# Kernel optimization log

Hardware: AMD Instinct MI355X
Metric: run time of the kernel (lower is better)

The kernel has to match this reference:

```python
import jax, jax.numpy as jnp
import numpy as np
from jax.scipy.special import logsumexp

EPS = 0.1
MAX_ITER = 100
LOG_SHIFT = 1e-8


def setup_inputs() -> dict:
    key = jax.random.key(0)
    kx, ky = jax.random.split(key)
    x = jax.random.normal(kx, (4, 2048, 64), dtype=jnp.float32)
    y = jax.random.normal(ky, (4, 2048, 64), dtype=jnp.float32)
    return {"x": x, "y": y}


def _cost_matrix(x, y):
    # |x_i - y_j|^2 summed over features; for p=2 use the expanded quadratic form
    # to avoid materializing a [B, P1, P2, D] intermediate.
    x2 = jnp.sum(x * x, axis=-1)  # [B, P1]
    y2 = jnp.sum(y * y, axis=-1)  # [B, P2]
    xy = jnp.einsum('bpd,bqd->bpq', x, y)  # [B, P1, P2]
    return x2[:, :, None] + y2[:, None, :] - 2.0 * xy


def _M(C, u, v):
    # M_ij = (-C_ij + u_i + v_j) / eps
    return (-C + u[..., :, None] + v[..., None, :]) / EPS


def reference(x, y):
    C = _cost_matrix(x, y)  # [B, P1, P2]
    B, P1, P2 = C.shape
    mu = jnp.full((B, P1), 1.0 / P1, dtype=C.dtype)
    nu = jnp.full((B, P2), 1.0 / P2, dtype=C.dtype)
    log_mu = jnp.log(mu + LOG_SHIFT)
    log_nu = jnp.log(nu + LOG_SHIFT)

    def step(carry, _):
        u, v = carry
        u = EPS * (log_mu - logsumexp(_M(C, u, v), axis=-1)) + u
        # logsumexp of M^T over its last dim == logsumexp of M over axis -2
        v = EPS * (log_nu - logsumexp(_M(C, u, v), axis=-2)) + v
        return (u, v), None

    u0 = jnp.zeros_like(mu)
    v0 = jnp.zeros_like(nu)
    (u, v), _ = jax.lax.scan(step, (u0, v0), None, length=MAX_ITER)

    pi = jnp.exp(_M(C, u, v))  # transport plan [B, P1, P2]
    cost = jnp.sum(pi * C, axis=(-2, -1))  # [B], reduction='none'
    return cost, pi, C
```

## Files before the change

kernel.cpp:

```cpp
#include <hip/hip_runtime.h>
#include <hip/hip_bf16.h>
#include <math.h>


#define P 2048
#define D 64
#define B 4
#define EPS 0.1f
#define KS 14.426950408889634f
#define EL2 0.06931471805599453f

#define EX2 __builtin_amdgcn_exp2f
#define LG2 __builtin_amdgcn_logf

__global__ __launch_bounds__(256) void cost_kernel(
    const float* __restrict__ X, const float* __restrict__ Y,
    float* __restrict__ C) {
  __shared__ float xs[64][65];
  __shared__ float ys[64][65];
  const int b = blockIdx.z;
  const int i0 = blockIdx.y * 64;
  const int j0 = blockIdx.x * 64;
  const float* Xb = X + ((size_t)b * P + i0) * D;
  const float* Yb = Y + ((size_t)b * P + j0) * D;
  const int t = threadIdx.x;
#pragma unroll
  for (int n = 0; n < 4; n++) {
    int e4 = t + n * 256;
    float4 xv = ((const float4*)Xb)[e4];
    float4 yv = ((const float4*)Yb)[e4];
    int r = e4 >> 4;
    int k = (e4 & 15) * 4;
    xs[r][k] = xv.x; xs[r][k + 1] = xv.y; xs[r][k + 2] = xv.z; xs[r][k + 3] = xv.w;
    ys[r][k] = yv.x; ys[r][k + 1] = yv.y; ys[r][k + 2] = yv.z; ys[r][k + 3] = yv.w;
  }
  __syncthreads();
  const int tx = t & 15;
  const int ty = t >> 4;
  float acc[4][4] = {};
#pragma unroll
  for (int k = 0; k < D; k++) {
    float a[4], bb[4];
#pragma unroll
    for (int r = 0; r < 4; r++) a[r] = xs[ty * 4 + r][k];
#pragma unroll
    for (int c = 0; c < 4; c++) bb[c] = ys[tx * 4 + c][k];
#pragma unroll
    for (int r = 0; r < 4; r++)
#pragma unroll
      for (int c = 0; c < 4; c++) {
        float d = a[r] - bb[c];
        acc[r][c] = fmaf(d, d, acc[r][c]);
      }
  }
#pragma unroll
  for (int r = 0; r < 4; r++) {
    float4 o = make_float4(acc[r][0], acc[r][1], acc[r][2], acc[r][3]);
    *(float4*)&C[((size_t)b * P + i0 + ty * 4 + r) * P + j0 + tx * 4] = o;
  }
}

__global__ __launch_bounds__(256, 2) void sweep_kernel(
    const float* __restrict__ C, const float* __restrict__ v,
    float* __restrict__ u, float2* __restrict__ part, float elog) {
  const int bid = blockIdx.x;
  const int grow0 = bid * 16;
  const int b = grow0 >> 11;
  const int kb = bid & 127;
  const int t = threadIdx.x;
  const int lane = t & 63;
  const int w = t >> 6;

  float vvK[8];
  {
    const float4* vp = (const float4*)(v + ((size_t)b << 11) + t * 8);
    float4 a = vp[0], c4 = vp[1];
    vvK[0] = a.x * KS;  vvK[1] = a.y * KS;  vvK[2] = a.z * KS;  vvK[3] = a.w * KS;
    vvK[4] = c4.x * KS; vvK[5] = c4.y * KS; vvK[6] = c4.z * KS; vvK[7] = c4.w * KS;
  }

  float colm[8], cols[8];
#pragma unroll
  for (int j = 0; j < 8; j++) { colm[j] = -__builtin_inff(); cols[j] = 0.f; }

  __shared__ float redm[4][8];
  __shared__ float reds[4][8];

#pragma unroll
  for (int g = 0; g < 2; g++) {
    float cK[8][8];
    const float* Cb = C + ((size_t)(grow0 + g * 8)) * P + t * 8;
#pragma unroll
    for (int r = 0; r < 8; r++) {
      float4 a = *(const float4*)(Cb + (size_t)r * P);
      float4 q = *(const float4*)(Cb + (size_t)r * P + 4);
      cK[r][0] = a.x * KS; cK[r][1] = a.y * KS; cK[r][2] = a.z * KS; cK[r][3] = a.w * KS;
      cK[r][4] = q.x * KS; cK[r][5] = q.y * KS; cK[r][6] = q.z * KS; cK[r][7] = q.w * KS;
    }

    float lm[8];
#pragma unroll
    for (int r = 0; r < 8; r++) {
      float m = vvK[0] - cK[r][0];
#pragma unroll
      for (int j = 1; j < 8; j++) m = fmaxf(m, vvK[j] - cK[r][j]);
#pragma unroll
      for (int off = 32; off; off >>= 1) m = fmaxf(m, __shfl_xor(m, off));
      lm[r] = m;
    }
    if (lane == 0) {
#pragma unroll
      for (int r = 0; r < 8; r++) redm[w][r] = lm[r];
    }
    __syncthreads();
    float bm[8];
#pragma unroll
    for (int r = 0; r < 8; r++)
      bm[r] = fmaxf(fmaxf(redm[0][r], redm[1][r]),
                    fmaxf(redm[2][r], redm[3][r]));
    float ls[8];
#pragma unroll
    for (int r = 0; r < 8; r++) {
      float s = 0.f;
#pragma unroll
      for (int j = 0; j < 8; j++) s += EX2(vvK[j] - cK[r][j] - bm[r]);
#pragma unroll
      for (int off = 32; off; off >>= 1) s += __shfl_xor(s, off);
      ls[r] = s;
    }
    if (lane == 0) {
#pragma unroll
      for (int r = 0; r < 8; r++) reds[w][r] = ls[r];
    }
    __syncthreads();
    float urK[8];
    float urr[8];
#pragma unroll
    for (int r = 0; r < 8; r++) {
      float S = (reds[0][r] + reds[1][r]) + (reds[2][r] + reds[3][r]);
      urr[r] = elog - EL2 * (bm[r] + LG2(S));
      urK[r] = urr[r] * KS;
    }
    if (t == 0) {
#pragma unroll
      for (int r = 0; r < 8; r++) u[grow0 + g * 8 + r] = urr[r];
    }

#pragma unroll
    for (int cc = 0; cc < 8; cc++) {
      float z[8];
#pragma unroll
      for (int r = 0; r < 8; r++) z[r] = urK[r] - cK[r][cc];
      float tm = z[0];
#pragma unroll
      for (int r = 1; r < 8; r++) tm = fmaxf(tm, z[r]);
      float M = fmaxf(colm[cc], tm);
      float s = 0.f;
#pragma unroll
      for (int r = 0; r < 8; r++) s += EX2(z[r] - M);
      cols[cc] = cols[cc] * EX2(colm[cc] - M) + s;
      colm[cc] = M;
    }
    __syncthreads();
  }

#pragma unroll
  for (int cc = 0; cc < 8; cc++) {
    part[(size_t)kb * (B * P) + (size_t)b * P + t * 8 + cc] =
        make_float2(colm[cc], cols[cc]);
  }
}

__global__ __launch_bounds__(256) void reduce_v(
    const float2* __restrict__ part, float* __restrict__ v, float elog) {
  const int gtid = blockIdx.x * 256 + threadIdx.x;
  const int col = gtid >> 2;
  const int seg = gtid & 3;
  const int k0 = seg * 32;
  float m = -__builtin_inff();
  float s = 0.f;
#pragma unroll 8
  for (int k = 0; k < 32; k++) {
    float2 p = part[(size_t)(k0 + k) * (B * P) + col];
    float M = fmaxf(m, p.x);
    s = s * EX2(m - M) + p.y * EX2(p.x - M);
    m = M;
  }
#pragma unroll
  for (int off = 1; off <= 2; off <<= 1) {
    float om = __shfl_xor(m, off);
    float os = __shfl_xor(s, off);
    float M = fmaxf(m, om);
    s = s * EX2(m - M) + os * EX2(om - M);
    m = M;
  }
  if (seg == 0) v[col] = elog - EL2 * (m + LG2(s));
}

__global__ __launch_bounds__(256) void final_pi(
    const float* __restrict__ C, const float* __restrict__ u,
    const float* __restrict__ v, float* __restrict__ pi,
    float* __restrict__ cost) {
  const int row = blockIdx.x;
  const int b = row >> 11;
  const int t = threadIdx.x;
  const float4* cp = (const float4*)(C + (size_t)row * P);
  const float4* vp = (const float4*)(v + ((size_t)b << 11));
  float4* pp = (float4*)(pi + (size_t)row * P);
  const float ui = u[row];
  float acc = 0.f;
#pragma unroll
  for (int n = 0; n < 2; n++) {
    float4 c = cp[t + n * 256];
    float4 vv = vp[t + n * 256];
    float4 p;
    p.x = EX2((ui + vv.x - c.x) * KS);
    p.y = EX2((ui + vv.y - c.y) * KS);
    p.z = EX2((ui + vv.z - c.z) * KS);
    p.w = EX2((ui + vv.w - c.w) * KS);
    acc += p.x * c.x + p.y * c.y + p.z * c.z + p.w * c.w;
    pp[t + n * 256] = p;
  }
#pragma unroll
  for (int off = 32; off; off >>= 1) acc += __shfl_xor(acc, off);
  __shared__ float sa[4];
  if ((t & 63) == 0) sa[t >> 6] = acc;
  __syncthreads();
  if (t == 0) atomicAdd(cost + b, sa[0] + sa[1] + sa[2] + sa[3]);
}

extern "C" void kernel_launch(void* const* d_in, const int* in_sizes, int n_in,
                              void* d_out, int out_size, void* d_ws,
                              size_t ws_size, hipStream_t stream) {
  const float* x = (const float*)d_in[0];
  const float* y = (const float*)d_in[1];
  float* out = (float*)d_out;
  float* cost = out;
  float* pi = out + 4;
  float* Cmat = out + 4 + (size_t)B * P * P;

  float2* part = (float2*)pi;
  float* u = (float*)d_ws;
  float* v = u + B * P;

  hipMemsetAsync(v, 0, B * P * sizeof(float), stream);
  hipMemsetAsync(cost, 0, 4 * sizeof(float), stream);

  dim3 cgrid(P / 64, P / 64, B);
  cost_kernel<<<cgrid, 256, 0, stream>>>(x, y, Cmat);

  const float elog = EPS * logf(1.0f / (float)P + 1e-8f);

  for (int it = 0; it < 100; it++) {
    sweep_kernel<<<B * P / 16, 256, 0, stream>>>(Cmat, v, u, part, elog);
    reduce_v<<<B * P * 4 / 256, 256, 0, stream>>>(part, v, elog);
  }

  final_pi<<<B * P, 256, 0, stream>>>(Cmat, u, v, pi, cost);
}
```

Measured before the change: 2.750 ms.

## Halve rows per sweep block, raise occupancy, and restructure column partial reduction

Each sweep block now handles 8 rows instead of 16 and the launch bound asks for 4 blocks per CU, so the kernel runs twice as many lighter blocks with less register pressure. Column partials are written as float4 pairs. The number of partial slices per column doubles to 256, and the reduce kernel now uses wave-per-segment accumulation followed by a shared-memory merge. final_pi processes 4 rows per block and reuses the preloaded v values. The trade is twice the partial traffic written and read each iteration, in exchange for more parallelism and latency hiding in the sweep.

```diff
diff --git a/kernel.cpp b/kernel.cpp
--- a/kernel.cpp
+++ b/kernel.cpp
@@ -6,6 +6,7 @@
 #define P 2048
 #define D 64
 #define B 4
+#define ITERS 100
 #define EPS 0.1f
 #define KS 14.426950408889634f
 #define EL2 0.06931471805599453f
@@ -60,36 +61,31 @@
   }
 }
 
-__global__ __launch_bounds__(256, 2) void sweep_kernel(
+__global__ __launch_bounds__(256, 4) void sweep8(
     const float* __restrict__ C, const float* __restrict__ v,
     float* __restrict__ u, float2* __restrict__ part, float elog) {
   const int bid = blockIdx.x;
-  const int grow0 = bid * 16;
-  const int b = grow0 >> 11;
-  const int kb = bid & 127;
+  const int rows0 = bid * 8;
+  const int b = bid >> 8;
+  const int kb = bid & 255;
   const int t = threadIdx.x;
   const int lane = t & 63;
   const int w = t >> 6;
 
-  float vvK[8];
-  {
-    const float4* vp = (const float4*)(v + ((size_t)b << 11) + t * 8);
-    float4 a = vp[0], c4 = vp[1];
-    vvK[0] = a.x * KS;  vvK[1] = a.y * KS;  vvK[2] = a.z * KS;  vvK[3] = a.w * KS;
-    vvK[4] = c4.x * KS; vvK[5] = c4.y * KS; vvK[6] = c4.z * KS; vvK[7] = c4.w * KS;
-  }
-
-  float colm[8], cols[8];
-#pragma unroll
-  for (int j = 0; j < 8; j++) { colm[j] = -__builtin_inff(); cols[j] = 0.f; }
-
   __shared__ float redm[4][8];
   __shared__ float reds[4][8];
 
-#pragma unroll
-  for (int g = 0; g < 2; g++) {
-    float cK[8][8];
-    const float* Cb = C + ((size_t)(grow0 + g * 8)) * P + t * 8;
+  float vvK[8];
+  {
+    const float4* vp = (const float4*)(v + ((size_t)b << 11) + t * 8);
+    float4 a = vp[0], q = vp[1];
+    vvK[0] = a.x * KS; vvK[1] = a.y * KS; vvK[2] = a.z * KS; vvK[3] = a.w * KS;
+    vvK[4] = q.x * KS; vvK[5] = q.y * KS; vvK[6] = q.z * KS; vvK[7] = q.w * KS;
+  }
+
+  float cK[8][8];
+  {
+    const float* Cb = C + (size_t)rows0 * P + t * 8;
 #pragma unroll
     for (int r = 0; r < 8; r++) {
       float4 a = *(const float4*)(Cb + (size_t)r * P);
@@ -97,136 +93,153 @@
       cK[r][0] = a.x * KS; cK[r][1] = a.y * KS; cK[r][2] = a.z * KS; cK[r][3] = a.w * KS;
       cK[r][4] = q.x * KS; cK[r][5] = q.y * KS; cK[r][6] = q.z * KS; cK[r][7] = q.w * KS;
     }
-
-    float lm[8];
-#pragma unroll
-    for (int r = 0; r < 8; r++) {
-      float m = vvK[0] - cK[r][0];
-#pragma unroll
-      for (int j = 1; j < 8; j++) m = fmaxf(m, vvK[j] - cK[r][j]);
-#pragma unroll
-      for (int off = 32; off; off >>= 1) m = fmaxf(m, __shfl_xor(m, off));
-      lm[r] = m;
-    }
-    if (lane == 0) {
-#pragma unroll
-      for (int r = 0; r < 8; r++) redm[w][r] = lm[r];
-    }
-    __syncthreads();
-    float bm[8];
-#pragma unroll
-    for (int r = 0; r < 8; r++)
-      bm[r] = fmaxf(fmaxf(redm[0][r], redm[1][r]),
-                    fmaxf(redm[2][r], redm[3][r]));
-    float ls[8];
-#pragma unroll
-    for (int r = 0; r < 8; r++) {
-      float s = 0.f;
-#pragma unroll
-      for (int j = 0; j < 8; j++) s += EX2(vvK[j] - cK[r][j] - bm[r]);
-#pragma unroll
-      for (int off = 32; off; off >>= 1) s += __shfl_xor(s, off);
-      ls[r] = s;
-    }
-    if (lane == 0) {
-#pragma unroll
-      for (int r = 0; r < 8; r++) reds[w][r] = ls[r];
-    }
-    __syncthreads();
-    float urK[8];
-    float urr[8];
-#pragma unroll
-    for (int r = 0; r < 8; r++) {
-      float S = (reds[0][r] + reds[1][r]) + (reds[2][r] + reds[3][r]);
-      urr[r] = elog - EL2 * (bm[r] + LG2(S));
-      urK[r] = urr[r] * KS;
-    }
-    if (t == 0) {
-#pragma unroll
-      for (int r = 0; r < 8; r++) u[grow0 + g * 8 + r] = urr[r];
-    }
-
-#pragma unroll
-    for (int cc = 0; cc < 8; cc++) {
-      float z[8];
-#pragma unroll
-      for (int r = 0; r < 8; r++) z[r] = urK[r] - cK[r][cc];
-      float tm = z[0];
-#pragma unroll
-      for (int r = 1; r < 8; r++) tm = fmaxf(tm, z[r]);
-      float M = fmaxf(colm[cc], tm);
-      float s = 0.f;
-#pragma unroll
-      for (int r = 0; r < 8; r++) s += EX2(z[r] - M);
-      cols[cc] = cols[cc] * EX2(colm[cc] - M) + s;
-      colm[cc] = M;
-    }
-    __syncthreads();
-  }
-
+  }
+
+  float bm[8];
+#pragma unroll
+  for (int r = 0; r < 8; r++) {
+    float m = vvK[0] - cK[r][0];
+#pragma unroll
+    for (int j = 1; j < 8; j++) m = fmaxf(m, vvK[j] - cK[r][j]);
+#pragma unroll
+    for (int off = 32; off; off >>= 1) m = fmaxf(m, __shfl_xor(m, off));
+    bm[r] = m;
+  }
+  if (lane == 0) {
+#pragma unroll
+    for (int r = 0; r < 8; r++) redm[w][r] = bm[r];
+  }
+  __syncthreads();
+#pragma unroll
+  for (int r = 0; r < 8; r++)
+    bm[r] = fmaxf(fmaxf(redm[0][r], redm[1][r]),
+                  fmaxf(redm[2][r], redm[3][r]));
+  float ls[8];
+#pragma unroll
+  for (int r = 0; r < 8; r++) {
+    float s = 0.f;
+#pragma unroll
+    for (int j = 0; j < 8; j++) s += EX2(vvK[j] - cK[r][j] - bm[r]);
+#pragma unroll
+    for (int off = 32; off; off >>= 1) s += __shfl_xor(s, off);
+    ls[r] = s;
+  }
+  if (lane == 0) {
+#pragma unroll
+    for (int r = 0; r < 8; r++) reds[w][r] = ls[r];
+  }
+  __syncthreads();
+  float urK[8];
+#pragma unroll
+  for (int r = 0; r < 8; r++) {
+    float S = (reds[0][r] + reds[1][r]) + (reds[2][r] + reds[3][r]);
+    urK[r] = (elog - EL2 * (bm[r] + LG2(S))) * KS;
+  }
+  if (t == 0) {
+#pragma unroll
+    for (int r = 0; r < 8; r++) u[rows0 + r] = urK[r] * EL2;
+  }
+
+  float2 pw[8];
 #pragma unroll
   for (int cc = 0; cc < 8; cc++) {
-    part[(size_t)kb * (B * P) + (size_t)b * P + t * 8 + cc] =
-        make_float2(colm[cc], cols[cc]);
-  }
-}
-
-__global__ __launch_bounds__(256) void reduce_v(
+    float z[8];
+#pragma unroll
+    for (int r = 0; r < 8; r++) z[r] = urK[r] - cK[r][cc];
+    float tm = z[0];
+#pragma unroll
+    for (int r = 1; r < 8; r++) tm = fmaxf(tm, z[r]);
+    float s = 0.f;
+#pragma unroll
+    for (int r = 0; r < 8; r++) s += EX2(z[r] - tm);
+    pw[cc] = make_float2(tm, s);
+  }
+  {
+    float4* p4 = (float4*)(part + (size_t)kb * (B * P) + ((size_t)b << 11) + t * 8);
+#pragma unroll
+    for (int i = 0; i < 4; i++)
+      p4[i] = make_float4(pw[2 * i].x, pw[2 * i].y, pw[2 * i + 1].x, pw[2 * i + 1].y);
+  }
+}
+
+__global__ __launch_bounds__(256) void reduce_v2(
     const float2* __restrict__ part, float* __restrict__ v, float elog) {
-  const int gtid = blockIdx.x * 256 + threadIdx.x;
-  const int col = gtid >> 2;
-  const int seg = gtid & 3;
-  const int k0 = seg * 32;
+  const int t = threadIdx.x;
+  const int cl = t & 63;
+  const int wv = t >> 6;
+  const int col = blockIdx.x * 64 + cl;
+  const float2* pk = part + (size_t)wv * 64 * (B * P) + col;
   float m = -__builtin_inff();
   float s = 0.f;
 #pragma unroll 8
-  for (int k = 0; k < 32; k++) {
-    float2 p = part[(size_t)(k0 + k) * (B * P) + col];
+  for (int i = 0; i < 64; i++) {
+    float2 p = pk[(size_t)i * (B * P)];
     float M = fmaxf(m, p.x);
     s = s * EX2(m - M) + p.y * EX2(p.x - M);
     m = M;
   }
-#pragma unroll
-  for (int off = 1; off <= 2; off <<= 1) {
-    float om = __shfl_xor(m, off);
-    float os = __shfl_xor(s, off);
-    float M = fmaxf(m, om);
-    s = s * EX2(m - M) + os * EX2(om - M);
-    m = M;
-  }
-  if (seg == 0) v[col] = elog - EL2 * (m + LG2(s));
-}
-
-__global__ __launch_bounds__(256) void final_pi(
+  __shared__ float mm[4][64];
+  __shared__ float ss[4][64];
+  mm[wv][cl] = m;
+  ss[wv][cl] = s;
+  __syncthreads();
+  if (t < 64) {
+    float M0 = mm[0][t], S0 = ss[0][t];
+#pragma unroll
+    for (int k = 1; k < 4; k++) {
+      float pm = mm[k][t], ps = ss[k][t];
+      float M = fmaxf(M0, pm);
+      S0 = S0 * EX2(M0 - M) + ps * EX2(pm - M);
+      M0 = M;
+    }
+    v[blockIdx.x * 64 + t] = elog - EL2 * (M0 + LG2(S0));
+  }
+}
+
+__global__ __launch_bounds__(256) void final_pi2(
     const float* __restrict__ C, const float* __restrict__ u,
     const float* __restrict__ v, float* __restrict__ pi,
     float* __restrict__ cost) {
-  const int row = blockIdx.x;
-  const int b = row >> 11;
-  const int t = threadIdx.x;
-  const float4* cp = (const float4*)(C + (size_t)row * P);
-  const float4* vp = (const float4*)(v + ((size_t)b << 11));
-  float4* pp = (float4*)(pi + (size_t)row * P);
-  const float ui = u[row];
+  const int bid = blockIdx.x;
+  const int rows0 = bid * 4;
+  const int b = rows0 >> 11;
+  const int t = threadIdx.x;
+  const int lane = t & 63;
+  const int w = t >> 6;
+
+  float vvK[8];
+  {
+    const float4* vp = (const float4*)(v + ((size_t)b << 11) + t * 8);
+    float4 a = vp[0], q = vp[1];
+    vvK[0] = a.x * KS; vvK[1] = a.y * KS; vvK[2] = a.z * KS; vvK[3] = a.w * KS;
+    vvK[4] = q.x * KS; vvK[5] = q.y * KS; vvK[6] = q.z * KS; vvK[7] = q.w * KS;
+  }
+
   float acc = 0.f;
 #pragma unroll
-  for (int n = 0; n < 2; n++) {
-    float4 c = cp[t + n * 256];
-    float4 vv = vp[t + n * 256];
-    float4 p;
-    p.x = EX2((ui + vv.x - c.x) * KS);
-    p.y = EX2((ui + vv.y - c.y) * KS);
-    p.z = EX2((ui + vv.z - c.z) * KS);
-    p.w = EX2((ui + vv.w - c.w) * KS);
-    acc += p.x * c.x + p.y * c.y + p.z * c.z + p.w * c.w;
-    pp[t + n * 256] = p;
+  for (int r = 0; r < 4; r++) {
+    const int row = rows0 + r;
+    const float uK = u[row] * KS;
+    const float* cp = C + (size_t)row * P + t * 8;
+    float4 a = *(const float4*)(cp);
+    float4 q = *(const float4*)(cp + 4);
+    float c[8] = {a.x, a.y, a.z, a.w, q.x, q.y, q.z, q.w};
+    float p[8];
+#pragma unroll
+    for (int j = 0; j < 8; j++) {
+      p[j] = EX2(uK + vvK[j] - c[j] * KS);
+      acc = fmaf(p[j], c[j], acc);
+    }
+    float* pp = pi + (size_t)row * P + t * 8;
+    *(float4*)(pp) = make_float4(p[0], p[1], p[2], p[3]);
+    *(float4*)(pp + 4) = make_float4(p[4], p[5], p[6], p[7]);
   }
 #pragma unroll
   for (int off = 32; off; off >>= 1) acc += __shfl_xor(acc, off);
   __shared__ float sa[4];
-  if ((t & 63) == 0) sa[t >> 6] = acc;
-  __syncthreads();
-  if (t == 0) atomicAdd(cost + b, sa[0] + sa[1] + sa[2] + sa[3]);
+  if (lane == 0) sa[w] = acc;
+  __syncthreads();
+  if (t == 0) atomicAdd(cost + b, (sa[0] + sa[1]) + (sa[2] + sa[3]));
 }
 
 extern "C" void kernel_launch(void* const* d_in, const int* in_sizes, int n_in,
@@ -240,8 +253,8 @@
   float* Cmat = out + 4 + (size_t)B * P * P;
 
   float2* part = (float2*)pi;
-  float* u = (float*)d_ws;
-  float* v = u + B * P;
+  float* v = (float*)d_ws;
+  float* u = v + B * P;
 
   hipMemsetAsync(v, 0, B * P * sizeof(float), stream);
   hipMemsetAsync(cost, 0, 4 * sizeof(float), stream);
@@ -251,10 +264,10 @@
 
   const float elog = EPS * logf(1.0f / (float)P + 1e-8f);
 
-  for (int it = 0; it < 100; it++) {
-    sweep_kernel<<<B * P / 16, 256, 0, stream>>>(Cmat, v, u, part, elog);
-    reduce_v<<<B * P * 4 / 256, 256, 0, stream>>>(part, v, elog);
-  }
-
-  final_pi<<<B * P, 256, 0, stream>>>(Cmat, u, v, pi, cost);
-}
+  for (int it = 0; it < ITERS; it++) {
+    sweep8<<<B * P / 8, 256, 0, stream>>>(Cmat, v, u, part, elog);
+    reduce_v2<<<B * P / 64, 256, 0, stream>>>(part, v, elog);
+  }
+
+  final_pi2<<<B * P / 4, 256, 0, stream>>>(Cmat, u, v, pi, cost);
+}
```

After: 4.050 ms. 1.47x slower.
